# Kernel tuning notes

Measured on AMD Instinct MI355X. Metric: run time of the kernel, lower is better.

Reference implementation:

```python
import jax, jax.numpy as jnp
import numpy as np

NUM_MODELS = 64
IN_CHANNELS = 16
HIDDEN = 128
B, H, W = 16, 32, 32


def setup_inputs() -> dict:
    key = jax.random.key(0)
    k1, k2, k3, k4, k5 = jax.random.split(key, 5)
    M, C, Hd = NUM_MODELS, IN_CHANNELS, HIDDEN
    x = jax.random.normal(k1, (B, M * C, H, W), dtype=jnp.float32)
    # grouped 1x1 conv weights: per-group [out_per_group, in_per_group]
    w1 = jax.random.normal(k2, (M, Hd, 9 * C), dtype=jnp.float32) * 0.05
    b1 = jax.random.normal(k3, (M * Hd,), dtype=jnp.float32) * 0.05
    w2 = jax.random.normal(k4, (M, C, Hd), dtype=jnp.float32) * 0.05
    b2 = jax.random.normal(k5, (M * C,), dtype=jnp.float32) * 0.05
    return {"x": x, "w1": w1, "b1": b1, "w2": w2, "b2": b2}


def _perceive(x):
    # x: [B, M*C, H, W] -> [B, 9*M*C, H, W], order: center, then 8 shifts
    b, mc, h, w = x.shape
    padded = jnp.pad(x, ((0, 0), (0, 0), (1, 1), (1, 1)))
    shifts = [x]
    for r in (-1, 0, 1):
        for c in (-1, 0, 1):
            if r == 0 and c == 0:
                continue
            shifts.append(padded[:, :, r + 1:r + 1 + h, c + 1:c + 1 + w])
    return jnp.concatenate(shifts, axis=1)


def reference(x, w1, b1, w2, b2):
    M, C, Hd = NUM_MODELS, IN_CHANNELS, HIDDEN
    b, _, h, w = x.shape
    perception = _perceive(x)  # [B, 9*M*C, H, W]
    # grouped conv slices contiguous channel blocks of size 9*C per group
    per_g = perception.reshape(b, M, 9 * C, h, w)
    hdn = jnp.einsum('bmchw,mdc->bmdhw', per_g, w1) + b1.reshape(1, M, Hd, 1, 1)
    hdn = jax.nn.relu(hdn)
    dx = jnp.einsum('bmdhw,mcd->bmchw', hdn, w2) + b2.reshape(1, M, C, 1, 1)
    return x + dx.reshape(b, M * C, h, w)
```

## Files before the change

### kernel.cpp

```cpp
#include <hip/hip_runtime.h>
#include <hip/hip_bf16.h>


typedef __attribute__((ext_vector_type(8))) short short8;
typedef __attribute__((ext_vector_type(4))) float f32x4;

constexpr int Bn  = 16;
constexpr int Mn  = 64;
constexpr int Cn  = 16;
constexpr int Hd  = 128;
constexpr int K9  = 144;
constexpr int MCn = 1024;
constexpr int NP  = 128;
constexpr int PT_STRIDE = 304;
constexpr int HT_STRIDE = 272;
constexpr int NT  = 256;

constexpr size_t XPM_SLABS = 34 * 34;
constexpr size_t XPM_B     = XPM_SLABS * MCn;
constexpr size_t XPM_BYTES = (size_t)Bn * XPM_B * 2;
constexpr size_t W1_ELEMS  = (size_t)Mn * Hd * K9;
constexpr size_t W2_ELEMS  = (size_t)Mn * Cn * Hd;
constexpr size_t WS_NEED   = XPM_BYTES + 2 * (W1_ELEMS + W2_ELEMS);

__device__ __forceinline__ ushort f2bf(float f) {
    return __bfloat16_as_ushort(__float2bfloat16(f));
}
__device__ __forceinline__ float bf2f(ushort u) {
    union { uint i; float f; } v; v.i = (uint)u << 16; return v.f;
}

__global__ __launch_bounds__(256)
void prep_xpm(const float* __restrict__ x, ushort* __restrict__ xpm)
{
    const int bid = blockIdx.x;
    const int b  = bid >> 7;
    const int h  = (bid >> 2) & 31;
    const int ck = bid & 3;
    const int tid = threadIdx.x;

    __shared__ ushort T[256][36];

    const int mc = ck * 256 + tid;
    const float* src = x + (((size_t)b * MCn + mc) * 32 + h) * 32;
    #pragma unroll
    for (int j = 0; j < 8; ++j) {
        const float4 f = *(const float4*)(src + 4 * j);
        uint2 pk;
        pk.x = (uint)f2bf(f.x) | ((uint)f2bf(f.y) << 16);
        pk.y = (uint)f2bf(f.z) | ((uint)f2bf(f.w) << 16);
        *(uint2*)&T[tid][4 * j] = pk;
    }
    __syncthreads();

    ushort* const dstb = xpm + (size_t)b * XPM_B + ((size_t)(h + 1) * 34) * MCn
                       + ck * 256;
    #pragma unroll
    for (int rep = 0; rep < 4; ++rep) {
        const int q8 = tid & 31;
        const int w  = (tid >> 5) + 8 * rep;
        ushort tmp[8];
        #pragma unroll
        for (int k2 = 0; k2 < 8; ++k2) tmp[k2] = T[8 * q8 + k2][w];
        uint4 v;
        v.x = (uint)tmp[0] | ((uint)tmp[1] << 16);
        v.y = (uint)tmp[2] | ((uint)tmp[3] << 16);
        v.z = (uint)tmp[4] | ((uint)tmp[5] << 16);
        v.w = (uint)tmp[6] | ((uint)tmp[7] << 16);
        *(uint4*)(dstb + (size_t)(w + 1) * MCn + 8 * q8) = v;
    }
}

__global__ __launch_bounds__(128)
void prep_border(ushort* __restrict__ xpm)
{
    const int bp  = blockIdx.x;
    const int b   = bp / 132;
    const int pos = bp % 132;
    int hh, ww;
    if      (pos < 34)  { hh = 0;              ww = pos;        }
    else if (pos < 68)  { hh = 33;             ww = pos - 34;   }
    else if (pos < 100) { hh = pos - 68 + 1;   ww = 0;          }
    else                { hh = pos - 100 + 1;  ww = 33;         }
    ushort* dst = xpm + (size_t)b * XPM_B + ((size_t)hh * 34 + ww) * MCn
                + threadIdx.x * 8;
    *(uint4*)dst = (uint4){0, 0, 0, 0};
}

__global__ __launch_bounds__(256)
void prep_w(const float* __restrict__ w1, const float* __restrict__ w2,
            ushort* __restrict__ w1bf, ushort* __restrict__ w2bf)
{
    const size_t i = ((size_t)blockIdx.x * 256 + threadIdx.x) * 4;
    const float* src; ushort* dst; size_t e;
    if (i < W1_ELEMS) { src = w1; dst = w1bf; e = i; }
    else              { src = w2; dst = w2bf; e = i - W1_ELEMS; }
    const float4 f = *(const float4*)(src + e);
    uint2 pk;
    pk.x = (uint)f2bf(f.x) | ((uint)f2bf(f.y) << 16);
    pk.y = (uint)f2bf(f.z) | ((uint)f2bf(f.w) << 16);
    *(uint2*)(dst + e) = pk;
}

__global__ __launch_bounds__(NT, 4)
void nca_mfma_pm(const ushort* __restrict__ xpm,
                 const ushort* __restrict__ w1bf, const float* __restrict__ b1,
                 const ushort* __restrict__ w2bf, const float* __restrict__ b2,
                 float* __restrict__ out)
{
    __shared__ __align__(16) char U[NP * PT_STRIDE + 16];
    char* const PtL = U;
    char* const HtL = U;

    const int tid  = threadIdx.x;
    const int lane = tid & 63;
    const int wid  = tid >> 6;
    const int lr   = lane & 15;
    const int lk   = lane >> 4;

    const int bid = blockIdx.x;
    const int xcd = bid & 7;
    const int j   = bid >> 3;
    const int mlo = j & 31;
    const int glo = (j >> 5) & 15;
    const int mch = j >> 9;
    const int m   = mch * 32 + mlo;
    const int g   = glo * 8 + xcd;
    const int b   = g >> 3;
    const int p0  = (g & 7) * NP;

    const ushort* const xpb = xpm + (size_t)b * XPM_B;

    if (tid <= NP) {
        char* z = PtL + tid * PT_STRIDE + (tid < NP ? 288 : 0);
        *(int4*)z = (int4){0, 0, 0, 0};
    }

    short8 a1[2][5];
    #pragma unroll
    for (int rt = 0; rt < 2; ++rt) {
        const int row = wid * 32 + rt * 16 + lr;
        const ushort* wr = w1bf + (m * Hd + row) * K9;
        #pragma unroll
        for (int ks = 0; ks < 5; ++ks) {
            const int k0 = ks * 32 + lk * 8;
            a1[rt][ks] = (k0 < K9) ? *(const short8*)(wr + k0)
                                   : (short8){0,0,0,0,0,0,0,0};
        }
    }
    short8 a2[4];
    #pragma unroll
    for (int ks = 0; ks < 4; ++ks)
        a2[ks] = *(const short8*)(w2bf + (m * Cn + lr) * Hd + ks * 32 + lk * 8);

    {
        const unsigned long long TAB = 0xA62918405ull;
        const int ch0  = m * K9;
        const int s0g  = ch0 >> 10;
        const int mc0  = ch0 & 1023;
        const int len0 = min(K9, 1024 - mc0);
        const uint nib0 = (uint)(TAB >> (4 * s0g)) & 15u;
        const uint nib1 = (uint)(TAB >> (4 * (s0g + 1))) & 15u;
        const int dr0 = (int)(nib0 & 3u) - 1, dc0 = (int)(nib0 >> 2) - 1;
        const int dr1 = (int)(nib1 & 3u) - 1, dc1 = (int)(nib1 >> 2) - 1;

        const int p   = tid >> 1;
        const int c0c = (tid & 1) * 72;
        const int gp  = p0 + p;
        const int h   = gp >> 5, w = gp & 31;
        const ushort* src0 = xpb + ((h + dr0 + 1) * 34 + (w + dc0 + 1)) * MCn + mc0;
        const ushort* src1 = xpb + ((h + dr1 + 1) * 34 + (w + dc1 + 1)) * MCn;
        char* const dstb = PtL + p * PT_STRIDE + c0c * 2;

        #pragma unroll
        for (int i = 0; i < 9; ++i) {
            const int ko = c0c + 8 * i;
            const ushort* s = (ko < len0) ? (src0 + ko) : (src1 + (ko - len0));
            *(uint4*)(dstb + 16 * i) = *(const uint4*)s;
        }
    }
    __syncthreads();

    f32x4 acc[2][8];
    #pragma unroll
    for (int i = 0; i < 2; ++i)
        #pragma unroll
        for (int jj = 0; jj < 8; ++jj) acc[i][jj] = (f32x4){0.f, 0.f, 0.f, 0.f};

    #pragma unroll
    for (int ct = 0; ct < 8; ++ct) {
        const int p = ct * 16 + lr;
        const char* base = PtL + p * PT_STRIDE + lk * 16;
        short8 bfrag[5];
        #pragma unroll
        for (int ks = 0; ks < 5; ++ks)
            bfrag[ks] = *(const short8*)(base + ks * 64);
        #pragma unroll
        for (int ks = 0; ks < 5; ++ks) {
            acc[0][ct] = __builtin_amdgcn_mfma_f32_16x16x32_bf16(a1[0][ks], bfrag[ks], acc[0][ct], 0, 0, 0);
            acc[1][ct] = __builtin_amdgcn_mfma_f32_16x16x32_bf16(a1[1][ks], bfrag[ks], acc[1][ct], 0, 0, 0);
        }
    }
    __syncthreads();

    #pragma unroll
    for (int rt = 0; rt < 2; ++rt) {
        const int hd0 = wid * 32 + rt * 16 + lk * 4;
        const float4 bs = *(const float4*)(b1 + m * Hd + hd0);
        #pragma unroll
        for (int ct = 0; ct < 8; ++ct) {
            const int p = ct * 16 + lr;
            const f32x4 v = acc[rt][ct];
            uint2 pk;
            pk.x = (uint)f2bf(fmaxf(v[0] + bs.x, 0.f)) |
                   ((uint)f2bf(fmaxf(v[1] + bs.y, 0.f)) << 16);
            pk.y = (uint)f2bf(fmaxf(v[2] + bs.z, 0.f)) |
                   ((uint)f2bf(fmaxf(v[3] + bs.w, 0.f)) << 16);
            *(uint2*)(HtL + p * HT_STRIDE + hd0 * 2) = pk;
        }
    }
    __syncthreads();

    f32x4 acc2[2];
    #pragma unroll
    for (int jj = 0; jj < 2; ++jj) {
        const int ct = wid * 2 + jj;
        const int p  = ct * 16 + lr;
        const char* base = HtL + p * HT_STRIDE + lk * 16;
        short8 bb[4];
        #pragma unroll
        for (int ks = 0; ks < 4; ++ks)
            bb[ks] = *(const short8*)(base + ks * 64);
        f32x4 a = (f32x4){0.f, 0.f, 0.f, 0.f};
        #pragma unroll
        for (int ks = 0; ks < 4; ++ks)
            a = __builtin_amdgcn_mfma_f32_16x16x32_bf16(a2[ks], bb[ks], a, 0, 0, 0);
        acc2[jj] = a;
    }
    __syncthreads();

    const float4 b2v = *(const float4*)(b2 + m * Cn + lk * 4);
    float (*dxT)[132] = (float(*)[132])U;
    {
        const float bsv[4] = {b2v.x, b2v.y, b2v.z, b2v.w};
        #pragma unroll
        for (int jj = 0; jj < 2; ++jj) {
            const int px = (wid * 2 + jj) * 16 + lr;
            const int gp = p0 + px;
            const int h  = gp >> 5, w = gp & 31;
            const ushort* res = xpb + ((h + 1) * 34 + (w + 1)) * MCn + m * Cn + lk * 4;
            #pragma unroll
            for (int rr2 = 0; rr2 < 4; ++rr2)
                dxT[lk * 4 + rr2][px] = acc2[jj][rr2] + bsv[rr2] + bf2f(res[rr2]);
        }
    }
    __syncthreads();
    {
        const int c = tid >> 4, iq = tid & 15;
        const int px0 = 8 * iq;
        const float4 d0 = *(const float4*)&dxT[c][px0];
        const float4 d1 = *(const float4*)&dxT[c][px0 + 4];
        const size_t idx = ((size_t)(b * MCn + m * Cn + c)) * 1024 + p0 + px0;
        *(float4*)(out + idx)     = d0;
        *(float4*)(out + idx + 4) = d1;
    }
}

__global__ __launch_bounds__(NT, 4)
void nca_mfma_f32src(const float* __restrict__ x,  const float* __restrict__ w1,
                     const float* __restrict__ b1, const float* __restrict__ w2,
                     const float* __restrict__ b2, float* __restrict__ out)
{
    __shared__ __align__(16) char U[NP * PT_STRIDE + 16];
    char* const PtL = U;
    char* const HtL = U;

    const int tid  = threadIdx.x;
    const int lane = tid & 63;
    const int wid  = tid >> 6;
    const int lr   = lane & 15;
    const int lk   = lane >> 4;

    const int bid = blockIdx.x;
    const int xcd = bid & 7;
    const int jb  = bid >> 3;
    const int m   = jb & 63;
    const int g   = (jb >> 6) * 8 + xcd;
    const int b   = g >> 3;
    const int p0  = (g & 7) * NP;

    if (tid <= NP) {
        char* z = PtL + tid * PT_STRIDE + (tid < NP ? 288 : 0);
        *(int4*)z = (int4){0, 0, 0, 0};
    }

    short8 a1[2][5];
    #pragma unroll
    for (int rt = 0; rt < 2; ++rt) {
        const int row = wid * 32 + rt * 16 + lr;
        const float* wr = w1 + (m * Hd + row) * K9;
        #pragma unroll
        for (int ks = 0; ks < 5; ++ks) {
            const int k0 = ks * 32 + lk * 8;
            short8 t;
            if (k0 < K9) {
                const float4 f0 = *(const float4*)(wr + k0);
                const float4 f1 = *(const float4*)(wr + k0 + 4);
                t[0] = (short)f2bf(f0.x); t[1] = (short)f2bf(f0.y);
                t[2] = (short)f2bf(f0.z); t[3] = (short)f2bf(f0.w);
                t[4] = (short)f2bf(f1.x); t[5] = (short)f2bf(f1.y);
                t[6] = (short)f2bf(f1.z); t[7] = (short)f2bf(f1.w);
            } else t = (short8){0,0,0,0,0,0,0,0};
            a1[rt][ks] = t;
        }
    }
    short8 a2[4];
    #pragma unroll
    for (int ks = 0; ks < 4; ++ks) {
        const float* wr = w2 + (m * Cn + lr) * Hd + ks * 32 + lk * 8;
        const float4 f0 = *(const float4*)(wr);
        const float4 f1 = *(const float4*)(wr + 4);
        short8 t;
        t[0] = (short)f2bf(f0.x); t[1] = (short)f2bf(f0.y);
        t[2] = (short)f2bf(f0.z); t[3] = (short)f2bf(f0.w);
        t[4] = (short)f2bf(f1.x); t[5] = (short)f2bf(f1.y);
        t[6] = (short)f2bf(f1.z); t[7] = (short)f2bf(f1.w);
        a2[ks] = t;
    }
    {
        const int s     = tid & 7;
        const int kpl   = (tid >> 3) & 7;
        const int r     = tid >> 6;
        const int rbase = (g & 7) * 4 + r;
        const float* xb = x + (size_t)b * (MCn * 1024);
        const unsigned long long TAB = 0xA62918405ull;
        #pragma unroll
        for (int it = 0; it < 9; ++it) {
            const int kp = it * 8 + kpl;
            float4 hv[2];
            #pragma unroll
            for (int half = 0; half < 2; ++half) {
                const int ch = m * K9 + kp * 2 + half;
                const int sh = ch >> 10;
                const int mc = ch & 1023;
                const uint nib = (uint)(TAB >> (4 * sh)) & 15u;
                const int dr = (int)(nib & 3u) - 1;
                const int dc = (int)(nib >> 2) - 1;
                const int row = rbase + dr;
                const int wb  = 4 * s + dc;
                const int wc  = min(max(wb, 0), 28);
                float4 f = {0.f, 0.f, 0.f, 0.f};
                if ((unsigned)row < 32u)
                    f = *(const float4*)(xb + (mc * 32 + row) * 32 + wc);
                if (wb < 0)       { f.w = f.z; f.z = f.y; f.y = f.x; f.x = 0.f; }
                else if (wb > 28) { f.x = f.y; f.y = f.z; f.z = f.w; f.w = 0.f; }
                hv[half] = f;
            }
            char* dst = PtL + (r * 32 + 4 * s) * PT_STRIDE + kp * 4;
            *(uint*)(dst)                 = (uint)f2bf(hv[0].x) | ((uint)f2bf(hv[1].x) << 16);
            *(uint*)(dst + PT_STRIDE)     = (uint)f2bf(hv[0].y) | ((uint)f2bf(hv[1].y) << 16);
            *(uint*)(dst + 2 * PT_STRIDE) = (uint)f2bf(hv[0].z) | ((uint)f2bf(hv[1].z) << 16);
            *(uint*)(dst + 3 * PT_STRIDE) = (uint)f2bf(hv[0].w) | ((uint)f2bf(hv[1].w) << 16);
        }
    }
    __syncthreads();

    f32x4 acc[2][8];
    #pragma unroll
    for (int i = 0; i < 2; ++i)
        #pragma unroll
        for (int jj = 0; jj < 8; ++jj) acc[i][jj] = (f32x4){0.f, 0.f, 0.f, 0.f};
    #pragma unroll
    for (int ct = 0; ct < 8; ++ct) {
        const int p = ct * 16 + lr;
        const char* base = PtL + p * PT_STRIDE + lk * 16;
        short8 bfrag[5];
        #pragma unroll
        for (int ks = 0; ks < 5; ++ks)
            bfrag[ks] = *(const short8*)(base + ks * 64);
        #pragma unroll
        for (int ks = 0; ks < 5; ++ks) {
            acc[0][ct] = __builtin_amdgcn_mfma_f32_16x16x32_bf16(a1[0][ks], bfrag[ks], acc[0][ct], 0, 0, 0);
            acc[1][ct] = __builtin_amdgcn_mfma_f32_16x16x32_bf16(a1[1][ks], bfrag[ks], acc[1][ct], 0, 0, 0);
        }
    }
    __syncthreads();
    #pragma unroll
    for (int rt = 0; rt < 2; ++rt) {
        const int hd0 = wid * 32 + rt * 16 + lk * 4;
        const float4 bs = *(const float4*)(b1 + m * Hd + hd0);
        #pragma unroll
        for (int ct = 0; ct < 8; ++ct) {
            const int p = ct * 16 + lr;
            const f32x4 v = acc[rt][ct];
            uint2 pk;
            pk.x = (uint)f2bf(fmaxf(v[0] + bs.x, 0.f)) |
                   ((uint)f2bf(fmaxf(v[1] + bs.y, 0.f)) << 16);
            pk.y = (uint)f2bf(fmaxf(v[2] + bs.z, 0.f)) |
                   ((uint)f2bf(fmaxf(v[3] + bs.w, 0.f)) << 16);
            *(uint2*)(HtL + p * HT_STRIDE + hd0 * 2) = pk;
        }
    }
    __syncthreads();
    f32x4 acc2[2];
    #pragma unroll
    for (int jj = 0; jj < 2; ++jj) {
        const int ct = wid * 2 + jj;
        const int p  = ct * 16 + lr;
        const char* base = HtL + p * HT_STRIDE + lk * 16;
        short8 bb[4];
        #pragma unroll
        for (int ks = 0; ks < 4; ++ks)
            bb[ks] = *(const short8*)(base + ks * 64);
        f32x4 a = (f32x4){0.f, 0.f, 0.f, 0.f};
        #pragma unroll
        for (int ks = 0; ks < 4; ++ks)
            a = __builtin_amdgcn_mfma_f32_16x16x32_bf16(a2[ks], bb[ks], a, 0, 0, 0);
        acc2[jj] = a;
    }
    const float4 b2v = *(const float4*)(b2 + m * Cn + lk * 4);
    const float bsv[4] = {b2v.x, b2v.y, b2v.z, b2v.w};
    #pragma unroll
    for (int jj = 0; jj < 2; ++jj) {
        const int ct = wid * 2 + jj;
        const int gp = p0 + ct * 16 + lr;
        #pragma unroll
        for (int r = 0; r < 4; ++r) {
            const int c   = lk * 4 + r;
            const size_t idx = ((size_t)(b * MCn + m * Cn + c)) * 1024 + gp;
            out[idx] = x[idx] + acc2[jj][r] + bsv[r];
        }
    }
}

extern "C" void kernel_launch(void* const* d_in, const int* in_sizes, int n_in,
                              void* d_out, int out_size, void* d_ws, size_t ws_size,
                              hipStream_t stream)
{
    const float* x  = (const float*)d_in[0];
    const float* w1 = (const float*)d_in[1];
    const float* b1 = (const float*)d_in[2];
    const float* w2 = (const float*)d_in[3];
    const float* b2 = (const float*)d_in[4];
    float* out = (float*)d_out;
    const int grid = Mn * (Bn * 1024 / NP);

    if (ws_size >= WS_NEED) {
        ushort* xpm  = (ushort*)d_ws;
        ushort* w1bf = (ushort*)((char*)d_ws + XPM_BYTES);
        ushort* w2bf = w1bf + W1_ELEMS;
        prep_xpm<<<Bn * 32 * 4, 256, 0, stream>>>(x, xpm);
        prep_border<<<Bn * 132, 128, 0, stream>>>(xpm);
        prep_w<<<(int)((W1_ELEMS + W2_ELEMS) / 4 / 256), 256, 0, stream>>>(w1, w2, w1bf, w2bf);
        nca_mfma_pm<<<grid, NT, 0, stream>>>(xpm, w1bf, b1, w2bf, b2, out);
    } else {
        nca_mfma_f32src<<<grid, NT, 0, stream>>>(x, w1, b1, w2, b2, out);
    }
}
```

Measured before the change: 143.2 us.

## Halve pixel tile per block, raise occupancy, merge border and weight prep kernels

```diff
diff --git a/kernel.cpp b/kernel.cpp
--- a/kernel.cpp
+++ b/kernel.cpp
@@ -11,7 +11,7 @@
 constexpr int Hd  = 128;
 constexpr int K9  = 144;
 constexpr int MCn = 1024;
-constexpr int NP  = 128;
+constexpr int NP  = 64;
 constexpr int PT_STRIDE = 304;
 constexpr int HT_STRIDE = 272;
 constexpr int NT  = 256;
@@ -22,6 +22,9 @@
 constexpr size_t W1_ELEMS  = (size_t)Mn * Hd * K9;
 constexpr size_t W2_ELEMS  = (size_t)Mn * Cn * Hd;
 constexpr size_t WS_NEED   = XPM_BYTES + 2 * (W1_ELEMS + W2_ELEMS);
+
+constexpr int NB_BORDER = Bn * 132;
+constexpr int NB_W      = (int)((W1_ELEMS + W2_ELEMS) / 4 / 256);
 
 __device__ __forceinline__ ushort f2bf(float f) {
     return __bfloat16_as_ushort(__float2bfloat16(f));
@@ -71,38 +74,38 @@
     }
 }
 
-__global__ __launch_bounds__(128)
-void prep_border(ushort* __restrict__ xpm)
+__global__ __launch_bounds__(256)
+void prep_aux(const float* __restrict__ w1, const float* __restrict__ w2,
+              ushort* __restrict__ w1bf, ushort* __restrict__ w2bf,
+              ushort* __restrict__ xpm)
 {
-    const int bp  = blockIdx.x;
-    const int b   = bp / 132;
-    const int pos = bp % 132;
-    int hh, ww;
-    if      (pos < 34)  { hh = 0;              ww = pos;        }
-    else if (pos < 68)  { hh = 33;             ww = pos - 34;   }
-    else if (pos < 100) { hh = pos - 68 + 1;   ww = 0;          }
-    else                { hh = pos - 100 + 1;  ww = 33;         }
-    ushort* dst = xpm + (size_t)b * XPM_B + ((size_t)hh * 34 + ww) * MCn
-                + threadIdx.x * 8;
-    *(uint4*)dst = (uint4){0, 0, 0, 0};
-}
-
-__global__ __launch_bounds__(256)
-void prep_w(const float* __restrict__ w1, const float* __restrict__ w2,
-            ushort* __restrict__ w1bf, ushort* __restrict__ w2bf)
-{
-    const size_t i = ((size_t)blockIdx.x * 256 + threadIdx.x) * 4;
-    const float* src; ushort* dst; size_t e;
-    if (i < W1_ELEMS) { src = w1; dst = w1bf; e = i; }
-    else              { src = w2; dst = w2bf; e = i - W1_ELEMS; }
-    const float4 f = *(const float4*)(src + e);
-    uint2 pk;
-    pk.x = (uint)f2bf(f.x) | ((uint)f2bf(f.y) << 16);
-    pk.y = (uint)f2bf(f.z) | ((uint)f2bf(f.w) << 16);
-    *(uint2*)(dst + e) = pk;
-}
-
-__global__ __launch_bounds__(NT, 4)
+    const int bid = blockIdx.x;
+    const int tid = threadIdx.x;
+    if (bid < NB_BORDER) {
+        const int b   = bid / 132;
+        const int pos = bid % 132;
+        int hh, ww;
+        if      (pos < 34)  { hh = 0;              ww = pos;        }
+        else if (pos < 68)  { hh = 33;             ww = pos - 34;   }
+        else if (pos < 100) { hh = pos - 68 + 1;   ww = 0;          }
+        else                { hh = pos - 100 + 1;  ww = 33;         }
+        ushort* dst = xpm + (size_t)b * XPM_B + ((size_t)hh * 34 + ww) * MCn
+                    + tid * 4;
+        *(uint2*)dst = (uint2){0, 0};
+    } else {
+        const size_t i = ((size_t)(bid - NB_BORDER) * 256 + tid) * 4;
+        const float* src; ushort* dst; size_t e;
+        if (i < W1_ELEMS) { src = w1; dst = w1bf; e = i; }
+        else              { src = w2; dst = w2bf; e = i - W1_ELEMS; }
+        const float4 f = *(const float4*)(src + e);
+        uint2 pk;
+        pk.x = (uint)f2bf(f.x) | ((uint)f2bf(f.y) << 16);
+        pk.y = (uint)f2bf(f.z) | ((uint)f2bf(f.w) << 16);
+        *(uint2*)(dst + e) = pk;
+    }
+}
+
+__global__ __launch_bounds__(NT, 8)
 void nca_mfma_pm(const ushort* __restrict__ xpm,
                  const ushort* __restrict__ w1bf, const float* __restrict__ b1,
                  const ushort* __restrict__ w2bf, const float* __restrict__ b2,
@@ -122,12 +125,12 @@
     const int xcd = bid & 7;
     const int j   = bid >> 3;
     const int mlo = j & 31;
-    const int glo = (j >> 5) & 15;
-    const int mch = j >> 9;
+    const int glo = (j >> 5) & 31;
+    const int mch = j >> 10;
     const int m   = mch * 32 + mlo;
     const int g   = glo * 8 + xcd;
-    const int b   = g >> 3;
-    const int p0  = (g & 7) * NP;
+    const int b   = g >> 4;
+    const int p0  = (g & 15) * NP;
 
     const ushort* const xpb = xpm + (size_t)b * XPM_B;
 
@@ -153,7 +156,7 @@
     for (int ks = 0; ks < 4; ++ks)
         a2[ks] = *(const short8*)(w2bf + (m * Cn + lr) * Hd + ks * 32 + lk * 8);
 
-    {
+    if (tid < 128) {
         const unsigned long long TAB = 0xA62918405ull;
         const int ch0  = m * K9;
         const int s0g  = ch0 >> 10;
@@ -181,14 +184,14 @@
     }
     __syncthreads();
 
-    f32x4 acc[2][8];
+    f32x4 acc[2][4];
     #pragma unroll
     for (int i = 0; i < 2; ++i)
         #pragma unroll
-        for (int jj = 0; jj < 8; ++jj) acc[i][jj] = (f32x4){0.f, 0.f, 0.f, 0.f};
-
-    #pragma unroll
-    for (int ct = 0; ct < 8; ++ct) {
+        for (int jj = 0; jj < 4; ++jj) acc[i][jj] = (f32x4){0.f, 0.f, 0.f, 0.f};
+
+    #pragma unroll
+    for (int ct = 0; ct < 4; ++ct) {
         const int p = ct * 16 + lr;
         const char* base = PtL + p * PT_STRIDE + lk * 16;
         short8 bfrag[5];
@@ -208,7 +211,7 @@
         const int hd0 = wid * 32 + rt * 16 + lk * 4;
         const float4 bs = *(const float4*)(b1 + m * Hd + hd0);
         #pragma unroll
-        for (int ct = 0; ct < 8; ++ct) {
+        for (int ct = 0; ct < 4; ++ct) {
             const int p = ct * 16 + lr;
             const f32x4 v = acc[rt][ct];
             uint2 pk;
@@ -221,11 +224,9 @@
     }
     __syncthreads();
 
-    f32x4 acc2[2];
-    #pragma unroll
-    for (int jj = 0; jj < 2; ++jj) {
-        const int ct = wid * 2 + jj;
-        const int p  = ct * 16 + lr;
+    f32x4 acc2;
+    {
+        const int p  = wid * 16 + lr;
         const char* base = HtL + p * HT_STRIDE + lk * 16;
         short8 bb[4];
         #pragma unroll
@@ -235,34 +236,29 @@
         #pragma unroll
         for (int ks = 0; ks < 4; ++ks)
             a = __builtin_amdgcn_mfma_f32_16x16x32_bf16(a2[ks], bb[ks], a, 0, 0, 0);
-        acc2[jj] = a;
+        acc2 = a;
     }
     __syncthreads();
 
     const float4 b2v = *(const float4*)(b2 + m * Cn + lk * 4);
-    float (*dxT)[132] = (float(*)[132])U;
+    float (*dxT)[NP + 4] = (float(*)[NP + 4])U;
     {
         const float bsv[4] = {b2v.x, b2v.y, b2v.z, b2v.w};
-        #pragma unroll
-        for (int jj = 0; jj < 2; ++jj) {
-            const int px = (wid * 2 + jj) * 16 + lr;
-            const int gp = p0 + px;
-            const int h  = gp >> 5, w = gp & 31;
-            const ushort* res = xpb + ((h + 1) * 34 + (w + 1)) * MCn + m * Cn + lk * 4;
-            #pragma unroll
-            for (int rr2 = 0; rr2 < 4; ++rr2)
-                dxT[lk * 4 + rr2][px] = acc2[jj][rr2] + bsv[rr2] + bf2f(res[rr2]);
-        }
+        const int px = wid * 16 + lr;
+        const int gp = p0 + px;
+        const int h  = gp >> 5, w = gp & 31;
+        const ushort* res = xpb + ((h + 1) * 34 + (w + 1)) * MCn + m * Cn + lk * 4;
+        #pragma unroll
+        for (int rr2 = 0; rr2 < 4; ++rr2)
+            dxT[lk * 4 + rr2][px] = acc2[rr2] + bsv[rr2] + bf2f(res[rr2]);
     }
     __syncthreads();
     {
         const int c = tid >> 4, iq = tid & 15;
-        const int px0 = 8 * iq;
+        const int px0 = 4 * iq;
         const float4 d0 = *(const float4*)&dxT[c][px0];
-        const float4 d1 = *(const float4*)&dxT[c][px0 + 4];
         const size_t idx = ((size_t)(b * MCn + m * Cn + c)) * 1024 + p0 + px0;
-        *(float4*)(out + idx)     = d0;
-        *(float4*)(out + idx + 4) = d1;
+        *(float4*)(out + idx) = d0;
     }
 }
 
@@ -271,7 +267,7 @@
                      const float* __restrict__ b1, const float* __restrict__ w2,
                      const float* __restrict__ b2, float* __restrict__ out)
 {
-    __shared__ __align__(16) char U[NP * PT_STRIDE + 16];
+    __shared__ __align__(16) char U[128 * PT_STRIDE + 16];
     char* const PtL = U;
     char* const HtL = U;
 
@@ -287,10 +283,10 @@
     const int m   = jb & 63;
     const int g   = (jb >> 6) * 8 + xcd;
     const int b   = g >> 3;
-    const int p0  = (g & 7) * NP;
-
-    if (tid <= NP) {
-        char* z = PtL + tid * PT_STRIDE + (tid < NP ? 288 : 0);
+    const int p0  = (g & 7) * 128;
+
+    if (tid <= 128) {
+        char* z = PtL + tid * PT_STRIDE + (tid < 128 ? 288 : 0);
         *(int4*)z = (int4){0, 0, 0, 0};
     }
 
@@ -443,17 +439,17 @@
     const float* w2 = (const float*)d_in[3];
     const float* b2 = (const float*)d_in[4];
     float* out = (float*)d_out;
-    const int grid = Mn * (Bn * 1024 / NP);
 
     if (ws_size >= WS_NEED) {
         ushort* xpm  = (ushort*)d_ws;
         ushort* w1bf = (ushort*)((char*)d_ws + XPM_BYTES);
         ushort* w2bf = w1bf + W1_ELEMS;
         prep_xpm<<<Bn * 32 * 4, 256, 0, stream>>>(x, xpm);
-        prep_border<<<Bn * 132, 128, 0, stream>>>(xpm);
-        prep_w<<<(int)((W1_ELEMS + W2_ELEMS) / 4 / 256), 256, 0, stream>>>(w1, w2, w1bf, w2bf);
+        prep_aux<<<NB_BORDER + NB_W, 256, 0, stream>>>(w1, w2, w1bf, w2bf, xpm);
+        const int grid = Mn * (Bn * 1024 / NP);
         nca_mfma_pm<<<grid, NT, 0, stream>>>(xpm, w1bf, b1, w2bf, b2, out);
     } else {
+        const int grid = Mn * (Bn * 1024 / 128);
         nca_mfma_f32src<<<grid, NT, 0, stream>>>(x, w1, b1, w2, b2, out);
     }
 }
```

Measured after the change: 305.3 us. 113% more time.
